# Optimization experiments

Hardware: AMD Instinct MI355X
Metric: run time of the kernel (lower is better)

The kernel has to match this reference:

```python
import jax, jax.numpy as jnp
import numpy as np

K_CHEB = 3  # Chebyshev order K -> K+1 basis matrices, gcn order = K


def setup_inputs() -> dict:
    key = jax.random.key(0)
    ks = jax.random.split(key, 7)
    B, N, T, Cin, Cout, ndim = 32, 512, 12, 64, 64, 40
    support_len = K_CHEB + 1
    cin_total = (K_CHEB * support_len + 1) * Cin  # (order*support_len+1)*c_in = 832
    x = jax.random.normal(ks[0], (B, N, T, Cin), jnp.float32)
    adj = (jax.random.uniform(ks[1], (N, N)) < 0.05).astype(jnp.float32)
    adjacency = jnp.maximum(adj, jnp.eye(N, dtype=jnp.float32))
    embedding = jax.random.uniform(ks[2], (N, ndim), dtype=jnp.float32)  # nn.init.uniform_
    W1 = jax.random.normal(ks[3], (ndim, ndim // 2), jnp.float32) * 0.3
    W2 = jax.random.normal(ks[4], (ndim, ndim // 2), jnp.float32) * 0.3
    mlp_w = jax.random.normal(ks[5], (Cout, cin_total), jnp.float32) / np.float32(np.sqrt(cin_total))
    mlp_b = jnp.zeros((Cout,), jnp.float32)
    return {"x": x, "adjacency": adjacency, "embedding": embedding,
            "W1": W1, "W2": W2, "mlp_w": mlp_w, "mlp_b": mlp_b}


def _cheb_kernels(adjacency, embedding, W1, W2):
    # adaptive adjacency: embedding mixed through column-softmaxed projections
    e1 = embedding @ jax.nn.softmax(W1, axis=0)
    e2 = embedding @ jax.nn.softmax(W2, axis=0)
    e1 = e1 / (jnp.linalg.norm(e1, axis=1, keepdims=True) + 1e-8)
    e2 = e2 / (jnp.linalg.norm(e2, axis=1, keepdims=True) + 1e-8)
    weight = e1 @ e2.T  # (N, N)
    A = jnp.where(adjacency > 0.0, weight + adjacency, jnp.asarray(9e-15, adjacency.dtype))
    # symmetric normalization: L = I - D^-1/2 A D^-1/2 ; Ls = (2/maxeig)*L - I with maxeig=2 -> Ls = -sym(A)
    d = 1.0 / jnp.sqrt(A.sum(axis=1))
    Ls = -(d[:, None] * A * d[None, :])
    I = jnp.eye(A.shape[0], dtype=A.dtype)
    kernels = [I, Ls]
    for _ in range(1, K_CHEB):  # Chebyshev recursion: T_{k+1} = 2 Ls T_k - T_{k-1}
        kernels.append(2.0 * (Ls @ kernels[-1]) - kernels[-2])
    return kernels  # K_CHEB + 1 matrices of (N, N)


def reference(x, adjacency, embedding, W1, W2, mlp_w, mlp_b):
    supports = _cheb_kernels(adjacency, embedding, W1, W2)
    xp = jnp.transpose(x, (0, 3, 1, 2))  # (B, Cin, N, T)
    out = [xp]
    for a in supports:
        x1 = jnp.einsum('bcvt,vw->bcwt', xp, a)
        out.append(x1)
        for _ in range(2, K_CHEB + 1):  # gcn order = K_CHEB
            x1 = jnp.einsum('bcvt,vw->bcwt', x1, a)
            out.append(x1)
    h = jnp.concatenate(out, axis=1)  # (B, 832, N, T)
    h = jnp.einsum('bcvt,oc->bovt', h, mlp_w) + mlp_b[None, :, None, None]  # 1x1 conv
    h = jnp.transpose(h, (0, 2, 3, 1))  # (B, N, T, Cout)
    return jax.nn.relu(h + x)  # conv_r is None (Cin == Cout), dropout eval no-op
```

## Files before the change

### kernel.cpp

```cpp
#include <hip/hip_runtime.h>
#include <hip/hip_bf16.h>

typedef unsigned short ushortT;
typedef unsigned int uintT;
typedef __attribute__((ext_vector_type(8))) short bf16x8;
typedef __attribute__((ext_vector_type(4))) float f32x4;
typedef __attribute__((ext_vector_type(4))) unsigned short us4;

__device__ __forceinline__ ushortT f2bf(float f) {
    union { float f; uintT u; } x; x.f = f;
    uintT r = x.u + 0x7fffu + ((x.u >> 16) & 1u);
    return (ushortT)(r >> 16);
}
__device__ __forceinline__ float bf2f(ushortT u) {
    union { uintT u; float f; } x; x.u = ((uintT)u) << 16; return x.f;
}

#define ZLD 520

__global__ __launch_bounds__(256) void k_embed(const float* __restrict__ emb,
                                               const float* __restrict__ W1,
                                               const float* __restrict__ W2,
                                               float* __restrict__ e1,
                                               float* __restrict__ e2) {
    __shared__ float sW[800];
    __shared__ float sWs[800];
    const float* W = (blockIdx.x == 0) ? W1 : W2;
    float* e = (blockIdx.x == 0) ? e1 : e2;
    int tid = threadIdx.x;
    for (int i = tid; i < 800; i += 256) sW[i] = W[i];
    __syncthreads();
    if (tid < 20) {
        float mx = -1e30f;
        for (int i = 0; i < 40; ++i) mx = fmaxf(mx, sW[i * 20 + tid]);
        float s = 0.f;
        for (int i = 0; i < 40; ++i) s += __expf(sW[i * 20 + tid] - mx);
        float inv = 1.f / s;
        for (int i = 0; i < 40; ++i) sWs[i * 20 + tid] = __expf(sW[i * 20 + tid] - mx) * inv;
    }
    __syncthreads();
    for (int row = tid; row < 512; row += 256) {
        float acc[20];
        #pragma unroll
        for (int j = 0; j < 20; ++j) acc[j] = 0.f;
        for (int i = 0; i < 40; ++i) {
            float ev = emb[row * 40 + i];
            #pragma unroll
            for (int j = 0; j < 20; ++j) acc[j] += ev * sWs[i * 20 + j];
        }
        float s = 0.f;
        #pragma unroll
        for (int j = 0; j < 20; ++j) s += acc[j] * acc[j];
        float scale = 1.f / (sqrtf(s) + 1e-8f);
        #pragma unroll
        for (int j = 0; j < 20; ++j) e[row * 20 + j] = acc[j] * scale;
    }
}

__global__ __launch_bounds__(256) void k_adj(const float* __restrict__ adj,
                                             const float* __restrict__ e1,
                                             const float* __restrict__ e2,
                                             float* __restrict__ A,
                                             float* __restrict__ d) {
    int v = blockIdx.x, tid = threadIdx.x;
    __shared__ float ev[20];
    if (tid < 20) ev[tid] = e1[v * 20 + tid];
    __syncthreads();
    float local = 0.f;
    for (int w = tid; w < 512; w += 256) {
        float dot = 0.f;
        #pragma unroll
        for (int j = 0; j < 20; ++j) dot += ev[j] * e2[w * 20 + j];
        float av = adj[v * 512 + w];
        float Av = (av > 0.f) ? (dot + av) : 9e-15f;
        A[v * 512 + w] = Av;
        local += Av;
    }
    __shared__ float red[256];
    red[tid] = local;
    __syncthreads();
    for (int s = 128; s > 0; s >>= 1) {
        if (tid < s) red[tid] += red[tid + s];
        __syncthreads();
    }
    if (tid == 0) d[v] = 1.f / sqrtf(red[0]);
}

__global__ __launch_bounds__(256) void k_m(const float* __restrict__ A,
                                           const float* __restrict__ d,
                                           ushortT* __restrict__ P) {
    int w = blockIdx.x, tid = threadIdx.x;
    float dw = d[w];
    for (int v = tid; v < 512; v += 256) {
        float val = -d[v] * dw * A[v * 512 + w];
        P[512 * 512 + w * 512 + v] = f2bf(val);
    }
}

__global__ __launch_bounds__(256) void k_prep(const float* __restrict__ x,
                                              ushortT* __restrict__ xbf,
                                              const float* __restrict__ mlp_w,
                                              ushortT* __restrict__ Wq) {
    int bx = blockIdx.x;
    if (bx < 160) {
        int idx = bx * 256 + threadIdx.x;
        if (idx >= 10 * 64 * 64) return;
        int q = idx >> 12, rem = idx & 4095, o = rem >> 6, c = rem & 63;
        float v;
        if (q == 0) {
            v = 0.f;
            #pragma unroll
            for (int k = 0; k < 4; ++k) v += mlp_w[o * 832 + k * 64 + c];
        } else {
            v = mlp_w[o * 832 + (q + 3) * 64 + c];
        }
        Wq[idx] = f2bf(v);
    } else {
        size_t i = (size_t)(bx - 160) * 256 + threadIdx.x;
        int c = (int)(i & 15) * 4;
        int v = (int)((i >> 4) & 511);
        int bt = (int)(i >> 13);
        int b = bt / 12, t = bt - b * 12;
        f32x4 f = *(const f32x4*)(x + (((size_t)b * 512 + v) * 12 + t) * 64 + c);
        us4 o = { f2bf(f[0]), f2bf(f[1]), f2bf(f[2]), f2bf(f[3]) };
        *(us4*)(xbf + ((size_t)bt * 512 + v) * 64 + c) = o;
    }
}

__global__ __launch_bounds__(256) void k_gemm512(const ushortT* __restrict__ A,
                                                 const ushortT* __restrict__ B,
                                                 ushortT* __restrict__ out1,
                                                 ushortT* __restrict__ out2,
                                                 int mode,
                                                 const ushortT* __restrict__ aux,
                                                 const ushortT* __restrict__ A2,
                                                 const ushortT* __restrict__ B2,
                                                 ushortT* __restrict__ out3) {
    int bx = blockIdx.x;
    if (bx >= 64) { A = A2; B = B2; out1 = out3; out2 = nullptr; mode = 0; bx -= 64; }
    int wave = threadIdx.x >> 6, lane = threadIdx.x & 63;
    int lr = lane & 15, lg = lane >> 4;
    int mbase = (bx >> 3) * 64;
    int nbase = (bx & 7) * 64 + wave * 16;
    f32x4 acc[4] = {};
    for (int kk = 0; kk < 16; ++kk) {
        int k0 = kk * 32 + lg * 8;
        bf16x8 bfr;
        #pragma unroll
        for (int j = 0; j < 8; ++j) bfr[j] = (short)B[(k0 + j) * 512 + nbase + lr];
        #pragma unroll
        for (int wt = 0; wt < 4; ++wt) {
            bf16x8 af = *(const bf16x8*)(A + (mbase + wt * 16 + lr) * 512 + k0);
            acc[wt] = __builtin_amdgcn_mfma_f32_16x16x32_bf16(af, bfr, acc[wt], 0, 0, 0);
        }
    }
    #pragma unroll
    for (int wt = 0; wt < 4; ++wt)
        #pragma unroll
        for (int r = 0; r < 4; ++r) {
            int row = mbase + wt * 16 + lg * 4 + r;
            int col = nbase + lr;
            float v = acc[wt][r];
            out1[row * 512 + col] = f2bf(v);
            if (mode == 1) out2[row * 512 + col] = f2bf(2.f * v - (row == col ? 1.f : 0.f));
            else if (mode == 2) out2[row * 512 + col] = f2bf(4.f * v - 3.f * bf2f(aux[row * 512 + col]));
        }
}

template<bool XBF>
__global__ __launch_bounds__(512, 2) void k_main(const float* __restrict__ x,
                                                 const ushortT* __restrict__ xbf,
                                                 const ushortT* __restrict__ P,
                                                 const ushortT* __restrict__ Wq,
                                                 const float* __restrict__ bias,
                                                 float* __restrict__ out) {
    __shared__ ushortT Zt[64 * ZLD];
    const int SZ = 512 * 512;
    int bid = blockIdx.x;
    int b = bid / 24, rr = bid % 24, tt = rr >> 1, half = rr & 1;
    int tid = threadIdx.x, wave = tid >> 6, lane = tid & 63;
    int lr = lane & 15, lg = lane >> 4;
    int wbase = half * 256 + wave * 32;
    int vbase = wave * 64;

    const ushortT* xq = xbf + ((size_t)(b * 12 + tt) * 512 + vbase) * 64;
    const float*   xqf = x + ((size_t)(b * 512 + vbase) * 12 + tt) * 64;

    f32x4 oacc[2][4] = {};
    bf16x8 a0r[4], a1r[4];
    {
        const ushortT* pq1 = P + (size_t)SZ + (size_t)(wbase + lr) * 512 + lg * 8;
        #pragma unroll
        for (int s = 0; s < 4; ++s) {
            a0r[s] = *(const bf16x8*)(pq1 + s * 32);
            a1r[s] = *(const bf16x8*)(pq1 + 8192 + s * 32);
        }
    }

    for (int q = 0; q <= 9; ++q) {
        const ushortT* wqp = Wq + q * 4096;
        #pragma unroll
        for (int h = 0; h < 2; ++h) {
            bf16x8 xf[4];
            #pragma unroll
            for (int j = 0; j < 2; ++j) {
                int vrow = (h * 2 + j) * 16 + lr;
                if (XBF) {
                    xf[j * 2 + 0] = *(const bf16x8*)(xq + vrow * 64 + lg * 8);
                    xf[j * 2 + 1] = *(const bf16x8*)(xq + vrow * 64 + 32 + lg * 8);
                } else {
                    const float* px = xqf + (size_t)vrow * 768 + lg * 8;
                    f32x4 f0 = *(const f32x4*)px;
                    f32x4 f1 = *(const f32x4*)(px + 4);
                    f32x4 f2 = *(const f32x4*)(px + 32);
                    f32x4 f3 = *(const f32x4*)(px + 36);
                    bf16x8 v0, v1;
                    v0[0] = (short)f2bf(f0[0]); v0[1] = (short)f2bf(f0[1]);
                    v0[2] = (short)f2bf(f0[2]); v0[3] = (short)f2bf(f0[3]);
                    v0[4] = (short)f2bf(f1[0]); v0[5] = (short)f2bf(f1[1]);
                    v0[6] = (short)f2bf(f1[2]); v0[7] = (short)f2bf(f1[3]);
                    v1[0] = (short)f2bf(f2[0]); v1[1] = (short)f2bf(f2[1]);
                    v1[2] = (short)f2bf(f2[2]); v1[3] = (short)f2bf(f2[3]);
                    v1[4] = (short)f2bf(f3[0]); v1[5] = (short)f2bf(f3[1]);
                    v1[6] = (short)f2bf(f3[2]); v1[7] = (short)f2bf(f3[3]);
                    xf[j * 2 + 0] = v0;
                    xf[j * 2 + 1] = v1;
                }
            }
            #pragma unroll
            for (int ot = 0; ot < 4; ++ot) {
                int o = ot * 16 + lr;
                bf16x8 wf0 = *(const bf16x8*)(wqp + o * 64 + lg * 8);
                bf16x8 wf1 = *(const bf16x8*)(wqp + o * 64 + 32 + lg * 8);
                f32x4 z0 = {}, z1 = {};
                z0 = __builtin_amdgcn_mfma_f32_16x16x32_bf16(xf[0], wf0, z0, 0, 0, 0);
                z0 = __builtin_amdgcn_mfma_f32_16x16x32_bf16(xf[1], wf1, z0, 0, 0, 0);
                z1 = __builtin_amdgcn_mfma_f32_16x16x32_bf16(xf[2], wf0, z1, 0, 0, 0);
                z1 = __builtin_amdgcn_mfma_f32_16x16x32_bf16(xf[3], wf1, z1, 0, 0, 0);
                int zb = o * ZLD;
                {
                    int v0i = vbase + (h * 2 + 0) * 16 + lg * 4;
                    us4 pk = { f2bf(z0[0]), f2bf(z0[1]), f2bf(z0[2]), f2bf(z0[3]) };
                    *(us4*)&Zt[zb + v0i] = pk;
                }
                {
                    int v0i = vbase + (h * 2 + 1) * 16 + lg * 4;
                    us4 pk = { f2bf(z1[0]), f2bf(z1[1]), f2bf(z1[2]), f2bf(z1[3]) };
                    *(us4*)&Zt[zb + v0i] = pk;
                }
            }
        }
        __syncthreads();

        if (q == 0) {
            #pragma unroll
            for (int wt = 0; wt < 2; ++wt)
                #pragma unroll
                for (int ot = 0; ot < 4; ++ot) {
                    int o = ot * 16 + lr;
                    int w0 = wbase + wt * 16 + lg * 4;
                    us4 z4 = *(const us4*)&Zt[o * ZLD + w0];
                    oacc[wt][ot][0] = bf2f(z4[0]);
                    oacc[wt][ot][1] = bf2f(z4[1]);
                    oacc[wt][ot][2] = bf2f(z4[2]);
                    oacc[wt][ot][3] = bf2f(z4[3]);
                }
        } else {
            const ushortT* pq  = P + (size_t)q * SZ + (size_t)(wbase + lr) * 512 + lg * 8;
            const ushortT* pqn = pq + SZ;
            #pragma unroll
            for (int kk = 0; kk < 16; ++kk) {
                const int slot = kk & 3;
                int vb = kk * 32 + lg * 8;
                bf16x8 b0 = *(const bf16x8*)&Zt[(0 * 16 + lr) * ZLD + vb];
                bf16x8 b1 = *(const bf16x8*)&Zt[(1 * 16 + lr) * ZLD + vb];
                bf16x8 b2 = *(const bf16x8*)&Zt[(2 * 16 + lr) * ZLD + vb];
                bf16x8 b3 = *(const bf16x8*)&Zt[(3 * 16 + lr) * ZLD + vb];
                oacc[0][0] = __builtin_amdgcn_mfma_f32_16x16x32_bf16(a0r[slot], b0, oacc[0][0], 0, 0, 0);
                oacc[1][0] = __builtin_amdgcn_mfma_f32_16x16x32_bf16(a1r[slot], b0, oacc[1][0], 0, 0, 0);
                oacc[0][1] = __builtin_amdgcn_mfma_f32_16x16x32_bf16(a0r[slot], b1, oacc[0][1], 0, 0, 0);
                oacc[1][1] = __builtin_amdgcn_mfma_f32_16x16x32_bf16(a1r[slot], b1, oacc[1][1], 0, 0, 0);
                oacc[0][2] = __builtin_amdgcn_mfma_f32_16x16x32_bf16(a0r[slot], b2, oacc[0][2], 0, 0, 0);
                oacc[1][2] = __builtin_amdgcn_mfma_f32_16x16x32_bf16(a1r[slot], b2, oacc[1][2], 0, 0, 0);
                oacc[0][3] = __builtin_amdgcn_mfma_f32_16x16x32_bf16(a0r[slot], b3, oacc[0][3], 0, 0, 0);
                oacc[1][3] = __builtin_amdgcn_mfma_f32_16x16x32_bf16(a1r[slot], b3, oacc[1][3], 0, 0, 0);
                if (kk < 12) {
                    a0r[slot] = *(const bf16x8*)(pq + (kk + 4) * 32);
                    a1r[slot] = *(const bf16x8*)(pq + 8192 + (kk + 4) * 32);
                } else if (q < 9) {
                    a0r[slot] = *(const bf16x8*)(pqn + (kk - 12) * 32);
                    a1r[slot] = *(const bf16x8*)(pqn + 8192 + (kk - 12) * 32);
                }
            }
        }
        __syncthreads();
    }

    #pragma unroll
    for (int wt = 0; wt < 2; ++wt)
        #pragma unroll
        for (int ot = 0; ot < 4; ++ot)
            #pragma unroll
            for (int r = 0; r < 4; ++r) {
                int w = wbase + wt * 16 + lg * 4 + r;
                int o = ot * 16 + lr;
                size_t oi = (((size_t)b * 512 + w) * 12 + tt) * 64 + o;
                float v = oacc[wt][ot][r] + x[oi] + bias[o];
                out[oi] = (v > 0.f) ? v : 0.f;
            }
}

extern "C" void kernel_launch(void* const* d_in, const int* in_sizes, int n_in,
                              void* d_out, int out_size, void* d_ws, size_t ws_size,
                              hipStream_t stream) {
    const float* x    = (const float*)d_in[0];
    const float* adj  = (const float*)d_in[1];
    const float* emb  = (const float*)d_in[2];
    const float* W1   = (const float*)d_in[3];
    const float* W2   = (const float*)d_in[4];
    const float* mlpw = (const float*)d_in[5];
    const float* mlpb = (const float*)d_in[6];
    float* out = (float*)d_out;

    char* ws = (char*)d_ws;
    float*   e1   = (float*)(ws + 0);
    float*   e2   = (float*)(ws + 65536);
    float*   A    = (float*)(ws + 131072);
    float*   dvec = (float*)(ws + 1179648);
    ushortT* P    = (ushortT*)(ws + 1183744);
    ushortT* Wq   = (ushortT*)(ws + 6426624);
    ushortT* xbf  = (ushortT*)(ws + 6508544);
    const size_t WS_NEED = 6508544 + (size_t)32 * 12 * 512 * 64 * 2;
    const bool use_xbf = (ws_size >= WS_NEED);

    k_embed<<<2, 256, 0, stream>>>(emb, W1, W2, e1, e2);
    k_adj<<<512, 256, 0, stream>>>(adj, e1, e2, A, dvec);
    k_m<<<512, 256, 0, stream>>>(A, dvec, P);
    k_prep<<<use_xbf ? 12448 : 160, 256, 0, stream>>>(x, xbf, mlpw, Wq);

    const int SZ = 512 * 512;
    ushortT *S1 = P + 1 * SZ, *S2 = P + 2 * SZ, *S3 = P + 3 * SZ, *S4 = P + 4 * SZ,
            *S5 = P + 5 * SZ, *S6 = P + 6 * SZ, *S7 = P + 7 * SZ, *S8 = P + 8 * SZ,
            *S9 = P + 9 * SZ;
    k_gemm512<<<64, 256, 0, stream>>>(S1, S1, S2, S4, 1, nullptr, nullptr, nullptr, nullptr);
    k_gemm512<<<128, 256, 0, stream>>>(S1, S2, S3, S7, 2, S1, S4, S4, S5);
    k_gemm512<<<128, 256, 0, stream>>>(S4, S5, S6, nullptr, 0, nullptr, S7, S7, S8);
    k_gemm512<<<64, 256, 0, stream>>>(S7, S8, S9, nullptr, 0, nullptr, nullptr, nullptr, nullptr);

    if (use_xbf)
        k_main<true><<<768, 512, 0, stream>>>(x, xbf, P, Wq, mlpb, out);
    else
        k_main<false><<<768, 512, 0, stream>>>(x, nullptr, P, Wq, mlpb, out);
    (void)in_sizes; (void)n_in; (void)out_size;
}
```

Baseline: 391.8 us.

## Split Z staging into two 256-node chunks to halve LDS footprint

The per-block Z tile in LDS is halved (ZLD 520→264) by computing the x·W projection in two 256-node chunks, each followed by its own P-matmul pass, instead of one full 512-node tile. The aim is to cut LDS use so more blocks can be resident per CU. The register prefetch ring of P fragments is removed in favour of direct loads inside the loop, and s_setprio is raised around the MFMA phase. This adds an extra barrier pair per q iteration and exposes more global-load latency on P.

```diff
diff --git a/kernel.cpp b/kernel.cpp
--- a/kernel.cpp
+++ b/kernel.cpp
@@ -16,7 +16,7 @@
     union { uintT u; float f; } x; x.u = ((uintT)u) << 16; return x.f;
 }
 
-#define ZLD 520
+#define ZLD 264
 
 __global__ __launch_bounds__(256) void k_embed(const float* __restrict__ emb,
                                                const float* __restrict__ W1,
@@ -181,119 +181,103 @@
     int tid = threadIdx.x, wave = tid >> 6, lane = tid & 63;
     int lr = lane & 15, lg = lane >> 4;
     int wbase = half * 256 + wave * 32;
-    int vbase = wave * 64;
-
-    const ushortT* xq = xbf + ((size_t)(b * 12 + tt) * 512 + vbase) * 64;
-    const float*   xqf = x + ((size_t)(b * 512 + vbase) * 12 + tt) * 64;
+    int vloc = wave * 32;
+
+    const ushortT* xq = xbf + (size_t)(b * 12 + tt) * 512 * 64;
+    const float*   xqf = x + ((size_t)b * 512 * 12 + tt) * 64;
 
     f32x4 oacc[2][4] = {};
-    bf16x8 a0r[4], a1r[4];
-    {
-        const ushortT* pq1 = P + (size_t)SZ + (size_t)(wbase + lr) * 512 + lg * 8;
-        #pragma unroll
-        for (int s = 0; s < 4; ++s) {
-            a0r[s] = *(const bf16x8*)(pq1 + s * 32);
-            a1r[s] = *(const bf16x8*)(pq1 + 8192 + s * 32);
-        }
-    }
-
-    for (int q = 0; q <= 9; ++q) {
+
+    auto zchunk = [&](int q, int ch) {
         const ushortT* wqp = Wq + q * 4096;
-        #pragma unroll
-        for (int h = 0; h < 2; ++h) {
-            bf16x8 xf[4];
+        int vb0 = ch * 256 + vloc;
+        bf16x8 xf[4];
+        #pragma unroll
+        for (int vt = 0; vt < 2; ++vt) {
+            int vrow = vb0 + vt * 16 + lr;
+            if (XBF) {
+                xf[vt * 2 + 0] = *(const bf16x8*)(xq + vrow * 64 + lg * 8);
+                xf[vt * 2 + 1] = *(const bf16x8*)(xq + vrow * 64 + 32 + lg * 8);
+            } else {
+                const float* px = xqf + (size_t)vrow * 768 + lg * 8;
+                f32x4 f0 = *(const f32x4*)px;
+                f32x4 f1 = *(const f32x4*)(px + 4);
+                f32x4 f2 = *(const f32x4*)(px + 32);
+                f32x4 f3 = *(const f32x4*)(px + 36);
+                bf16x8 v0, v1;
+                v0[0] = (short)f2bf(f0[0]); v0[1] = (short)f2bf(f0[1]);
+                v0[2] = (short)f2bf(f0[2]); v0[3] = (short)f2bf(f0[3]);
+                v0[4] = (short)f2bf(f1[0]); v0[5] = (short)f2bf(f1[1]);
+                v0[6] = (short)f2bf(f1[2]); v0[7] = (short)f2bf(f1[3]);
+                v1[0] = (short)f2bf(f2[0]); v1[1] = (short)f2bf(f2[1]);
+                v1[2] = (short)f2bf(f2[2]); v1[3] = (short)f2bf(f2[3]);
+                v1[4] = (short)f2bf(f3[0]); v1[5] = (short)f2bf(f3[1]);
+                v1[6] = (short)f2bf(f3[2]); v1[7] = (short)f2bf(f3[3]);
+                xf[vt * 2 + 0] = v0;
+                xf[vt * 2 + 1] = v1;
+            }
+        }
+        #pragma unroll
+        for (int ot = 0; ot < 4; ++ot) {
+            int o = ot * 16 + lr;
+            bf16x8 wf0 = *(const bf16x8*)(wqp + o * 64 + lg * 8);
+            bf16x8 wf1 = *(const bf16x8*)(wqp + o * 64 + 32 + lg * 8);
+            f32x4 z0 = {}, z1 = {};
+            z0 = __builtin_amdgcn_mfma_f32_16x16x32_bf16(xf[0], wf0, z0, 0, 0, 0);
+            z0 = __builtin_amdgcn_mfma_f32_16x16x32_bf16(xf[1], wf1, z0, 0, 0, 0);
+            z1 = __builtin_amdgcn_mfma_f32_16x16x32_bf16(xf[2], wf0, z1, 0, 0, 0);
+            z1 = __builtin_amdgcn_mfma_f32_16x16x32_bf16(xf[3], wf1, z1, 0, 0, 0);
+            int zb = o * ZLD + vloc + lg * 4;
+            us4 p0 = { f2bf(z0[0]), f2bf(z0[1]), f2bf(z0[2]), f2bf(z0[3]) };
+            *(us4*)&Zt[zb] = p0;
+            us4 p1 = { f2bf(z1[0]), f2bf(z1[1]), f2bf(z1[2]), f2bf(z1[3]) };
+            *(us4*)&Zt[zb + 16] = p1;
+        }
+    };
+
+    zchunk(0, half);
+    __syncthreads();
+    #pragma unroll
+    for (int wt = 0; wt < 2; ++wt)
+        #pragma unroll
+        for (int ot = 0; ot < 4; ++ot) {
+            int o = ot * 16 + lr;
+            us4 z4 = *(const us4*)&Zt[o * ZLD + vloc + wt * 16 + lg * 4];
+            oacc[wt][ot][0] = bf2f(z4[0]);
+            oacc[wt][ot][1] = bf2f(z4[1]);
+            oacc[wt][ot][2] = bf2f(z4[2]);
+            oacc[wt][ot][3] = bf2f(z4[3]);
+        }
+    __syncthreads();
+
+    for (int q = 1; q <= 9; ++q) {
+        const ushortT* pq = P + (size_t)q * SZ + (size_t)(wbase + lr) * 512 + lg * 8;
+        #pragma unroll
+        for (int ch = 0; ch < 2; ++ch) {
+            zchunk(q, ch);
+            __syncthreads();
+            __builtin_amdgcn_s_setprio(1);
             #pragma unroll
-            for (int j = 0; j < 2; ++j) {
-                int vrow = (h * 2 + j) * 16 + lr;
-                if (XBF) {
-                    xf[j * 2 + 0] = *(const bf16x8*)(xq + vrow * 64 + lg * 8);
-                    xf[j * 2 + 1] = *(const bf16x8*)(xq + vrow * 64 + 32 + lg * 8);
-                } else {
-                    const float* px = xqf + (size_t)vrow * 768 + lg * 8;
-                    f32x4 f0 = *(const f32x4*)px;
-                    f32x4 f1 = *(const f32x4*)(px + 4);
-                    f32x4 f2 = *(const f32x4*)(px + 32);
-                    f32x4 f3 = *(const f32x4*)(px + 36);
-                    bf16x8 v0, v1;
-                    v0[0] = (short)f2bf(f0[0]); v0[1] = (short)f2bf(f0[1]);
-                    v0[2] = (short)f2bf(f0[2]); v0[3] = (short)f2bf(f0[3]);
-                    v0[4] = (short)f2bf(f1[0]); v0[5] = (short)f2bf(f1[1]);
-                    v0[6] = (short)f2bf(f1[2]); v0[7] = (short)f2bf(f1[3]);
-                    v1[0] = (short)f2bf(f2[0]); v1[1] = (short)f2bf(f2[1]);
-                    v1[2] = (short)f2bf(f2[2]); v1[3] = (short)f2bf(f2[3]);
-                    v1[4] = (short)f2bf(f3[0]); v1[5] = (short)f2bf(f3[1]);
-                    v1[6] = (short)f2bf(f3[2]); v1[7] = (short)f2bf(f3[3]);
-                    xf[j * 2 + 0] = v0;
-                    xf[j * 2 + 1] = v1;
-                }
-            }
-            #pragma unroll
-            for (int ot = 0; ot < 4; ++ot) {
-                int o = ot * 16 + lr;
-                bf16x8 wf0 = *(const bf16x8*)(wqp + o * 64 + lg * 8);
-                bf16x8 wf1 = *(const bf16x8*)(wqp + o * 64 + 32 + lg * 8);
-                f32x4 z0 = {}, z1 = {};
-                z0 = __builtin_amdgcn_mfma_f32_16x16x32_bf16(xf[0], wf0, z0, 0, 0, 0);
-                z0 = __builtin_amdgcn_mfma_f32_16x16x32_bf16(xf[1], wf1, z0, 0, 0, 0);
-                z1 = __builtin_amdgcn_mfma_f32_16x16x32_bf16(xf[2], wf0, z1, 0, 0, 0);
-                z1 = __builtin_amdgcn_mfma_f32_16x16x32_bf16(xf[3], wf1, z1, 0, 0, 0);
-                int zb = o * ZLD;
-                {
-                    int v0i = vbase + (h * 2 + 0) * 16 + lg * 4;
-                    us4 pk = { f2bf(z0[0]), f2bf(z0[1]), f2bf(z0[2]), f2bf(z0[3]) };
-                    *(us4*)&Zt[zb + v0i] = pk;
-                }
-                {
-                    int v0i = vbase + (h * 2 + 1) * 16 + lg * 4;
-                    us4 pk = { f2bf(z1[0]), f2bf(z1[1]), f2bf(z1[2]), f2bf(z1[3]) };
-                    *(us4*)&Zt[zb + v0i] = pk;
-                }
-            }
-        }
-        __syncthreads();
-
-        if (q == 0) {
-            #pragma unroll
-            for (int wt = 0; wt < 2; ++wt)
-                #pragma unroll
-                for (int ot = 0; ot < 4; ++ot) {
-                    int o = ot * 16 + lr;
-                    int w0 = wbase + wt * 16 + lg * 4;
-                    us4 z4 = *(const us4*)&Zt[o * ZLD + w0];
-                    oacc[wt][ot][0] = bf2f(z4[0]);
-                    oacc[wt][ot][1] = bf2f(z4[1]);
-                    oacc[wt][ot][2] = bf2f(z4[2]);
-                    oacc[wt][ot][3] = bf2f(z4[3]);
-                }
-        } else {
-            const ushortT* pq  = P + (size_t)q * SZ + (size_t)(wbase + lr) * 512 + lg * 8;
-            const ushortT* pqn = pq + SZ;
-            #pragma unroll
-            for (int kk = 0; kk < 16; ++kk) {
-                const int slot = kk & 3;
+            for (int kk = 0; kk < 8; ++kk) {
+                bf16x8 a0 = *(const bf16x8*)(pq + ch * 256 + kk * 32);
+                bf16x8 a1 = *(const bf16x8*)(pq + 8192 + ch * 256 + kk * 32);
                 int vb = kk * 32 + lg * 8;
                 bf16x8 b0 = *(const bf16x8*)&Zt[(0 * 16 + lr) * ZLD + vb];
                 bf16x8 b1 = *(const bf16x8*)&Zt[(1 * 16 + lr) * ZLD + vb];
                 bf16x8 b2 = *(const bf16x8*)&Zt[(2 * 16 + lr) * ZLD + vb];
                 bf16x8 b3 = *(const bf16x8*)&Zt[(3 * 16 + lr) * ZLD + vb];
-                oacc[0][0] = __builtin_amdgcn_mfma_f32_16x16x32_bf16(a0r[slot], b0, oacc[0][0], 0, 0, 0);
-                oacc[1][0] = __builtin_amdgcn_mfma_f32_16x16x32_bf16(a1r[slot], b0, oacc[1][0], 0, 0, 0);
-                oacc[0][1] = __builtin_amdgcn_mfma_f32_16x16x32_bf16(a0r[slot], b1, oacc[0][1], 0, 0, 0);
-                oacc[1][1] = __builtin_amdgcn_mfma_f32_16x16x32_bf16(a1r[slot], b1, oacc[1][1], 0, 0, 0);
-                oacc[0][2] = __builtin_amdgcn_mfma_f32_16x16x32_bf16(a0r[slot], b2, oacc[0][2], 0, 0, 0);
-                oacc[1][2] = __builtin_amdgcn_mfma_f32_16x16x32_bf16(a1r[slot], b2, oacc[1][2], 0, 0, 0);
-                oacc[0][3] = __builtin_amdgcn_mfma_f32_16x16x32_bf16(a0r[slot], b3, oacc[0][3], 0, 0, 0);
-                oacc[1][3] = __builtin_amdgcn_mfma_f32_16x16x32_bf16(a1r[slot], b3, oacc[1][3], 0, 0, 0);
-                if (kk < 12) {
-                    a0r[slot] = *(const bf16x8*)(pq + (kk + 4) * 32);
-                    a1r[slot] = *(const bf16x8*)(pq + 8192 + (kk + 4) * 32);
-                } else if (q < 9) {
-                    a0r[slot] = *(const bf16x8*)(pqn + (kk - 12) * 32);
-                    a1r[slot] = *(const bf16x8*)(pqn + 8192 + (kk - 12) * 32);
-                }
+                oacc[0][0] = __builtin_amdgcn_mfma_f32_16x16x32_bf16(a0, b0, oacc[0][0], 0, 0, 0);
+                oacc[1][0] = __builtin_amdgcn_mfma_f32_16x16x32_bf16(a1, b0, oacc[1][0], 0, 0, 0);
+                oacc[0][1] = __builtin_amdgcn_mfma_f32_16x16x32_bf16(a0, b1, oacc[0][1], 0, 0, 0);
+                oacc[1][1] = __builtin_amdgcn_mfma_f32_16x16x32_bf16(a1, b1, oacc[1][1], 0, 0, 0);
+                oacc[0][2] = __builtin_amdgcn_mfma_f32_16x16x32_bf16(a0, b2, oacc[0][2], 0, 0, 0);
+                oacc[1][2] = __builtin_amdgcn_mfma_f32_16x16x32_bf16(a1, b2, oacc[1][2], 0, 0, 0);
+                oacc[0][3] = __builtin_amdgcn_mfma_f32_16x16x32_bf16(a0, b3, oacc[0][3], 0, 0, 0);
+                oacc[1][3] = __builtin_amdgcn_mfma_f32_16x16x32_bf16(a1, b3, oacc[1][3], 0, 0, 0);
             }
-        }
-        __syncthreads();
+            __builtin_amdgcn_s_setprio(0);
+            __syncthreads();
+        }
     }
 
     #pragma unroll
```

Result: slower. 414.0 us (+5.6%).
